# Kernel tuning notes

Hardware: AMD Instinct MI355X
Metric: run time of the kernel (lower is better)

## Reference

```python
import jax, jax.numpy as jnp
import numpy as np
from jax import lax

EPS = 1e-5

def _conv(x, w, b, pad):
    y = lax.conv_general_dilated(x, w, (1, 1), [(pad, pad), (pad, pad)],
                                 dimension_numbers=('NCHW', 'OIHW', 'NCHW'))
    return y + b[None, :, None, None]

def _bn(x, g, b, m, v):
    # eval-mode BatchNorm2d with running stats
    scale = g * lax.rsqrt(v + EPS)
    return x * scale[None, :, None, None] + (b - m * scale)[None, :, None, None]

def setup_inputs() -> dict:
    key = jax.random.key(0)
    ks = jax.random.split(key, 16)
    B, C, H, W = 16, 64, 128, 128
    C2 = 2 * C
    d = {}
    d['x'] = jax.random.normal(ks[0], (B, C, H, W), jnp.float32)
    # fc1: Conv2d(C,C,3,p=1) + BN(C)
    d['fc1_w'] = jax.random.normal(ks[1], (C, C, 3, 3), jnp.float32) * 0.05
    d['fc1_b'] = jax.random.normal(ks[2], (C,), jnp.float32) * 0.05
    d['bn1_g'] = jnp.ones((C,), jnp.float32)
    d['bn1_b'] = jnp.zeros((C,), jnp.float32)
    d['bn1_m'] = jax.random.normal(ks[3], (C,), jnp.float32) * 0.05
    d['bn1_v'] = jax.random.uniform(ks[4], (C,), jnp.float32) * 0.5 + 0.5
    # graph_conv.nn: Conv2d(2C,2C,1) + BN(2C) + GELU
    d['gc_w'] = jax.random.normal(ks[5], (C2, C2, 1, 1), jnp.float32) * 0.05
    d['gc_b'] = jax.random.normal(ks[6], (C2,), jnp.float32) * 0.05
    d['bng_g'] = jnp.ones((C2,), jnp.float32)
    d['bng_b'] = jnp.zeros((C2,), jnp.float32)
    d['bng_m'] = jax.random.normal(ks[7], (C2,), jnp.float32) * 0.05
    d['bng_v'] = jax.random.uniform(ks[8], (C2,), jnp.float32) * 0.5 + 0.5
    # fc2: Conv2d(2C,C,3,p=1) + BN(C)
    d['fc2_w'] = jax.random.normal(ks[9], (C, C2, 3, 3), jnp.float32) * 0.05
    d['fc2_b'] = jax.random.normal(ks[10], (C,), jnp.float32) * 0.05
    d['bn2_g'] = jnp.ones((C,), jnp.float32)
    d['bn2_b'] = jnp.zeros((C,), jnp.float32)
    d['bn2_m'] = jax.random.normal(ks[11], (C,), jnp.float32) * 0.05
    d['bn2_v'] = jax.random.uniform(ks[12], (C,), jnp.float32) * 0.5 + 0.5
    return d

def reference(x, fc1_w, fc1_b, bn1_g, bn1_b, bn1_m, bn1_v,
              gc_w, gc_b, bng_g, bng_b, bng_m, bng_v,
              fc2_w, fc2_b, bn2_g, bn2_b, bn2_m, bn2_v):
    # fc1
    h = _bn(_conv(x, fc1_w, fc1_b, 1), bn1_g, bn1_b, bn1_m, bn1_v)
    # MRConv4dSP: strided self-attention over superpatch tokens
    sel = h[:, :, ::4, ::4]                          # [B,C,h4,w4]
    B, C, h4, w4 = sel.shape
    q = sel.reshape(B, C, h4 * w4).transpose(0, 2, 1)  # [B,N,C]
    scale = C ** (-0.5)
    att = jax.nn.softmax(jnp.einsum('bnc,bmc->bnm', q, q) * scale, axis=-1)
    o = jnp.einsum('bnm,bmc->bnc', att, q)           # [B,N,C]
    o = o.transpose(0, 2, 1).reshape(B, C, h4, w4)
    o = jnp.repeat(jnp.repeat(o, 4, axis=2), 4, axis=3)
    g = jnp.concatenate([h, o], axis=1)              # [B,2C,H,W]
    g = jax.nn.gelu(_bn(_conv(g, gc_w, gc_b, 0), bng_g, bng_b, bng_m, bng_v),
                    approximate=False)
    # fc2 + residual (drop_path=0 -> identity)
    y = _bn(_conv(g, fc2_w, fc2_b, 1), bn2_g, bn2_b, bn2_m, bn2_v)
    return y + x
```

## Files before the change

kernel.cpp:

```cpp
#include <hip/hip_runtime.h>
#include <math.h>

#define EPSV 1e-5f

typedef __bf16 bf16;
using bf16x8 = __attribute__((ext_vector_type(8))) __bf16;
using bf16x4 = __attribute__((ext_vector_type(4))) __bf16;
using bf16x2 = __attribute__((ext_vector_type(2))) __bf16;
using f32x4  = __attribute__((ext_vector_type(4))) float;

static __device__ __forceinline__ f32x4 mfma16(bf16x8 a, bf16x8 b, f32x4 c) {
    return __builtin_amdgcn_mfma_f32_16x16x32_bf16(a, b, c, 0, 0, 0);
}
static __device__ __forceinline__ f32x4 zero4() {
    f32x4 z = {0.f, 0.f, 0.f, 0.f};
    return z;
}

typedef __attribute__((address_space(1))) const char g_char_t;
typedef __attribute__((address_space(3))) char lds_char_t;
static __device__ __forceinline__ void gll16(const void* g, void* l) {
    __builtin_amdgcn_global_load_lds((g_char_t*)g, (lds_char_t*)l, 16, 0, 0);
}

static __device__ __forceinline__ float gelu_f(float v) {
    float z = fabsf(v) * 0.70710678118f;
    float t = __builtin_amdgcn_rcpf(1.f + 0.3275911f * z);
    float poly = t * (0.254829592f + t * (-0.284496736f + t * (1.421413741f +
                 t * (-1.453152027f + t * 1.061405429f))));
    float e = __expf(-z * z);
    float erfv = copysignf(1.f - poly * e, v);
    return 0.5f * v * (1.f + erfv);
}

template<int CIN>
__global__ __launch_bounds__(256) void prep_conv_w(const float* __restrict__ w,
                                                   bf16* __restrict__ wt)
{
    int t = blockIdx.x * 256 + threadIdx.x;
    if (t >= 64 * CIN) return;
    int cout = t / CIN, ci = t - cout * CIN;
    int cci = ci >> 5, lg = (ci >> 3) & 3, j = ci & 7;
    int mi = cout >> 4, lix = cout & 15;
#pragma unroll
    for (int kgt = 0; kgt < 9; ++kgt) {
        float v = w[(size_t)t * 9 + kgt];
        wt[((((size_t)kgt * (CIN >> 5) + cci) * 4 + mi) * 64 + lg * 16 + lix) * 8 + j]
            = (bf16)v;
    }
}

__global__ __launch_bounds__(256) void prep_1x1_w(const float* __restrict__ w,
                                                  bf16* __restrict__ wt)
{
    int t = blockIdx.x * 256 + threadIdx.x;
    int cout = t >> 7, ci = t & 127;
    int ks = ci >> 5, lg = (ci >> 3) & 3, j = ci & 7;
    wt[(((size_t)(ks * 4 + lg) * 128) + cout) * 8 + j] = (bf16)w[t];
}

__global__ __launch_bounds__(256) void cvt_x_nhwc(const float* __restrict__ x,
                                                  bf16* __restrict__ xb,
                                                  float* __restrict__ zb)
{
    __shared__ float t_lds[64 * 68];
    const int bx = blockIdx.x;
    const int b  = blockIdx.y;
    const int y  = bx >> 1, x0 = (bx & 1) * 64;
    const int tid = threadIdx.x;

    if (bx == 0 && b == 0 && tid < 64)
        ((float4*)zb)[tid] = make_float4(0.f, 0.f, 0.f, 0.f);

    for (int f = tid; f < 64 * 16; f += 256) {
        int c = f >> 4, xu = f & 15;
        float4 v = *(const float4*)&x[((size_t)(b * 64 + c) << 14) + (y << 7) + x0 + xu * 4];
        t_lds[(xu * 4 + 0) * 68 + c] = v.x;
        t_lds[(xu * 4 + 1) * 68 + c] = v.y;
        t_lds[(xu * 4 + 2) * 68 + c] = v.z;
        t_lds[(xu * 4 + 3) * 68 + c] = v.w;
    }
    __syncthreads();
    for (int f = tid; f < 64 * 8; f += 256) {
        int xx = f >> 3, cu = f & 7;
        const float* p = &t_lds[xx * 68 + cu * 8];
        bf16x8 v;
#pragma unroll
        for (int j = 0; j < 8; ++j) v[j] = (bf16)p[j];
        *(bf16x8*)&xb[((size_t)((b * 128 + y) * 128) + x0 + xx) * 64 + cu * 8] = v;
    }
}

template<int CIN, int OUTMODE>
__global__ __launch_bounds__(512) void conv3x3_mfma(
    const bf16* __restrict__ in, const bf16* __restrict__ wt,
    const float* __restrict__ bias,
    const float* __restrict__ bg, const float* __restrict__ bb,
    const float* __restrict__ bm, const float* __restrict__ bv,
    const bf16* __restrict__ resid, const bf16* __restrict__ zb,
    void* __restrict__ outp)
{
    constexpr int NC = CIN >> 5;
    __shared__ bf16 in_lds[2][672 * 32];
    __shared__ bf16 w_lds[2][36 * 512];

    const int wg = blockIdx.x;
    const int v  = (wg & 7) * 64 + (wg >> 3);
    const int tile = v & 31, b = v >> 5;
    const int x0 = (tile & 1) * 64;
    const int y0 = (tile >> 1) * 8;
    const int tid  = threadIdx.x;
    const int wid  = tid >> 6;
    const int lane = tid & 63;
    const int lix  = lane & 15, lg = lane >> 4;

    int goff[6]; bool gok[6];
#pragma unroll
    for (int i = 0; i < 6; ++i) {
        int chunk = wid + 8 * i;
        int f = chunk * 64 + lane;
        int pix = f >> 2, u = f & 3;
        int sw = (pix & 3) ^ ((pix >> 2) & 3);
        int ug = u ^ sw;
        int iy = pix / 66, ix = pix - iy * 66;
        int gy = y0 + iy - 1, gx = x0 + ix - 1;
        gok[i]  = (chunk < 42) && (pix < 660) &&
                  (unsigned)gy < 128u && (unsigned)gx < 128u;
        goff[i] = ((b * 128 + gy) * 128 + gx) * CIN + ug * 8;
    }
    int rd[9];
#pragma unroll
    for (int kg = 0; kg < 3; ++kg)
#pragma unroll
        for (int t = 0; t < 3; ++t) {
            int pix0 = (wid + kg) * 66 + lix + t;
            int sw = (pix0 & 3) ^ ((pix0 >> 2) & 3);
            rd[kg * 3 + t] = pix0 * 32 + ((lg ^ sw) << 3);
        }

    f32x4 acc[4][4];
#pragma unroll
    for (int i = 0; i < 4; ++i)
#pragma unroll
        for (int j = 0; j < 4; ++j) acc[i][j] = zero4();

    auto issue_in = [&](int cci, int buf) {
#pragma unroll
        for (int i = 0; i < 6; ++i) {
            int chunk = wid + 8 * i;
            if (chunk < 42) {
                const void* src = gok[i] ? (const void*)(in + goff[i] + cci * 32)
                                         : (const void*)zb;
                gll16(src, (char*)&in_lds[buf][0] + chunk * 1024);
            }
        }
    };
    auto issue_w = [&](int cci, int buf) {
#pragma unroll
        for (int i = 0; i < 5; ++i) {
            int chunk = wid + 8 * i;
            if (chunk < 36) {
                const bf16* src = wt + ((size_t)(chunk >> 2) * NC + cci) * 2048
                                     + (chunk & 3) * 512 + lane * 8;
                gll16(src, (char*)&w_lds[buf][0] + chunk * 1024);
            }
        }
    };
    auto compute = [&](int buf) {
        bf16x8 afA[4], bfA[4], afB[4], bfB[4];
#pragma unroll
        for (int mi = 0; mi < 4; ++mi)
            afA[mi] = *(const bf16x8*)&w_lds[buf][(0 * 4 + mi) * 512 + lane * 8];
#pragma unroll
        for (int nj = 0; nj < 4; ++nj)
            bfA[nj] = *(const bf16x8*)&in_lds[buf][rd[0] + nj * 512];
#pragma unroll
        for (int kgt = 0; kgt < 9; ++kgt) {
            bf16x8* afC = (kgt & 1) ? afB : afA;
            bf16x8* bfC = (kgt & 1) ? bfB : bfA;
            bf16x8* afN = (kgt & 1) ? afA : afB;
            bf16x8* bfN = (kgt & 1) ? bfA : bfB;
            if (kgt < 8) {
#pragma unroll
                for (int mi = 0; mi < 4; ++mi)
                    afN[mi] = *(const bf16x8*)&w_lds[buf][((kgt + 1) * 4 + mi) * 512 + lane * 8];
#pragma unroll
                for (int nj = 0; nj < 4; ++nj)
                    bfN[nj] = *(const bf16x8*)&in_lds[buf][rd[kgt + 1] + nj * 512];
            }
            __builtin_amdgcn_sched_barrier(0);
#pragma unroll
            for (int nj = 0; nj < 4; ++nj)
#pragma unroll
                for (int mi = 0; mi < 4; ++mi)
                    acc[mi][nj] = mfma16(afC[mi], bfC[nj], acc[mi][nj]);
            __builtin_amdgcn_sched_barrier(0);
        }
    };

    issue_in(0, 0);
    issue_w(0, 0);
#pragma unroll 1
    for (int c = 0; c < NC; ++c) {
        if (c + 1 < NC) {
            issue_in(c + 1, (c + 1) & 1);
            issue_w(c + 1, (c + 1) & 1);
            if (wid < 2)      asm volatile("s_waitcnt vmcnt(11)" ::: "memory");
            else if (wid < 4) asm volatile("s_waitcnt vmcnt(10)" ::: "memory");
            else              asm volatile("s_waitcnt vmcnt(9)"  ::: "memory");
        } else {
            asm volatile("s_waitcnt vmcnt(0)" ::: "memory");
        }
        __builtin_amdgcn_s_barrier();
        __builtin_amdgcn_sched_barrier(0);
        compute(c & 1);
        __builtin_amdgcn_s_barrier();
    }

    if (OUTMODE == 0) {
        bf16* out = (bf16*)outp;
        bf16* stg = &in_lds[0][0];
#pragma unroll
        for (int mi = 0; mi < 4; ++mi) {
            float A[4], Bc[4];
#pragma unroll
            for (int r = 0; r < 4; ++r) {
                int c = mi * 16 + lg * 4 + r;
                float s = bg[c] * rsqrtf(bv[c] + EPSV);
                A[r]  = s;
                Bc[r] = bias[c] * s + bb[c] - bm[c] * s;
            }
#pragma unroll
            for (int nj = 0; nj < 4; ++nj) {
                int px = nj * 16 + lix;
                bf16x4 vv;
#pragma unroll
                for (int r = 0; r < 4; ++r)
                    vv[r] = (bf16)(acc[mi][nj][r] * A[r] + Bc[r]);
                *(bf16x4*)&stg[(wid * 64 + px) * 68 + mi * 16 + lg * 4] = vv;
            }
        }
        __syncthreads();
#pragma unroll
        for (int k = 0; k < 8; ++k) {
            int idx = k * 512 + tid;
            int row = idx >> 9, rem = idx & 511;
            int px = rem >> 3, cu = rem & 7;
            bf16x8 vv = *(const bf16x8*)&stg[(row * 64 + px) * 68 + cu * 8];
            *(bf16x8*)&out[((size_t)((b * 128 + y0 + row) * 128)
                            + x0 + px) * 64 + cu * 8] = vv;
        }
    } else {
        float* out = (float*)outp;
        const int gy = y0 + wid;
#pragma unroll
        for (int mi = 0; mi < 4; ++mi) {
            float A[4], Bc[4];
#pragma unroll
            for (int r = 0; r < 4; ++r) {
                int c = mi * 16 + lg * 4 + r;
                float s = bg[c] * rsqrtf(bv[c] + EPSV);
                A[r]  = s;
                Bc[r] = bias[c] * s + bb[c] - bm[c] * s;
            }
#pragma unroll
            for (int nj = 0; nj < 4; ++nj) {
                int px = x0 + nj * 16 + lix;
                bf16x4 rv = *(const bf16x4*)&resid[((size_t)((b * 128 + gy) * 128) + px) * 64
                                                   + mi * 16 + lg * 4];
#pragma unroll
                for (int r = 0; r < 4; ++r) {
                    int c = mi * 16 + lg * 4 + r;
                    size_t oi = ((size_t)(b * 64 + c) << 14) + (gy << 7) + px;
                    out[oi] = acc[mi][nj][r] * A[r] + Bc[r] + (float)rv[r];
                }
            }
        }
    }
}

__global__ __launch_bounds__(256) void gather_q(const bf16* __restrict__ h,
                                                bf16* __restrict__ q)
{
    int t = blockIdx.x * 256 + threadIdx.x;
    int cu = t & 7, n = (t >> 3) & 1023, b = t >> 13;
    int y = (n >> 5) << 2, x = (n & 31) << 2;
    bf16x8 v = *(const bf16x8*)&h[((size_t)((b * 128 + y) * 128 + x)) * 64 + cu * 8];
    *(bf16x8*)&q[((size_t)(b * 1024 + n)) * 64 + cu * 8] = v;
}

__global__ __launch_bounds__(256) void attn_fused(const bf16* __restrict__ q,
                                                  bf16* __restrict__ o)
{
    __shared__ bf16 qn[64 * 72];
    __shared__ bf16 kn[128 * 72];
    __shared__ bf16 vt[64 * 136];
    __shared__ bf16 pl[4][16 * 136];
    __shared__ __align__(16) float fac[4][16];
    const int n0 = blockIdx.x * 64, b = blockIdx.y;
    const int tid = threadIdx.x, w = tid >> 6, lane = tid & 63;
    const int lix = lane & 15, lg = lane >> 4;
    const bf16* qb = q + ((size_t)b << 16);

    for (int f = tid; f < 512; f += 256) {
        int row = f >> 3, cu = f & 7;
        *(bf16x8*)&qn[row * 72 + cu * 8] =
            *(const bf16x8*)&qb[(size_t)(n0 + row) * 64 + cu * 8];
    }

    float m_run = -3.0e38f, l_run = 0.f;
    f32x4 oacc[4];
#pragma unroll
    for (int ct = 0; ct < 4; ++ct) oacc[ct] = zero4();

    for (int mt = 0; mt < 1024; mt += 128) {
        __syncthreads();
        for (int f = tid; f < 1024; f += 256) {
            int row = f >> 3, cu = f & 7;
            *(bf16x8*)&kn[row * 72 + cu * 8] =
                *(const bf16x8*)&qb[(size_t)(mt + row) * 64 + cu * 8];
        }
        for (int f = tid; f < 512; f += 256) {
            int mp = f >> 3, cu = f & 7;
            int m = mp * 2;
            bf16x8 a = *(const bf16x8*)&qb[(size_t)(mt + m) * 64 + cu * 8];
            bf16x8 c = *(const bf16x8*)&qb[(size_t)(mt + m + 1) * 64 + cu * 8];
#pragma unroll
            for (int j = 0; j < 8; ++j) {
                bf16x2 pr = {a[j], c[j]};
                *(bf16x2*)&vt[(cu * 8 + j) * 136 + m] = pr;
            }
        }
        __syncthreads();

        bf16x8 bq0 = *(const bf16x8*)&qn[(w * 16 + lix) * 72 + lg * 8];
        bf16x8 bq1 = *(const bf16x8*)&qn[(w * 16 + lix) * 72 + 32 + lg * 8];

        f32x4 s[8];
#pragma unroll
        for (int t = 0; t < 8; ++t) {
            bf16x8 a0 = *(const bf16x8*)&kn[(t * 16 + lix) * 72 + lg * 8];
            bf16x8 a1 = *(const bf16x8*)&kn[(t * 16 + lix) * 72 + 32 + lg * 8];
            s[t] = mfma16(a0, bq0, zero4());
            s[t] = mfma16(a1, bq1, s[t]);
        }

        float mx = -3.0e38f;
#pragma unroll
        for (int t = 0; t < 8; ++t)
#pragma unroll
            for (int r = 0; r < 4; ++r) { s[t][r] *= 0.125f; mx = fmaxf(mx, s[t][r]); }
        mx = fmaxf(mx, __shfl_xor(mx, 16));
        mx = fmaxf(mx, __shfl_xor(mx, 32));
        float m_new = fmaxf(m_run, mx);
        float alpha = __expf(m_run - m_new);

        float psum = 0.f;
#pragma unroll
        for (int t = 0; t < 8; ++t) {
            float p0 = __expf(s[t][0] - m_new), p1 = __expf(s[t][1] - m_new);
            float p2 = __expf(s[t][2] - m_new), p3 = __expf(s[t][3] - m_new);
            psum += (p0 + p1) + (p2 + p3);
            bf16x2 v01 = {(bf16)p0, (bf16)p1};
            bf16x2 v23 = {(bf16)p2, (bf16)p3};
            *(bf16x2*)&pl[w][lix * 136 + t * 16 + lg * 4]     = v01;
            *(bf16x2*)&pl[w][lix * 136 + t * 16 + lg * 4 + 2] = v23;
        }
        psum += __shfl_xor(psum, 16);
        psum += __shfl_xor(psum, 32);
        l_run = l_run * alpha + psum;
        m_run = m_new;
        if (lg == 0) fac[w][lix] = alpha;

        float4 a4 = *(const float4*)&fac[w][lg * 4];
        float aa[4] = {a4.x, a4.y, a4.z, a4.w};
#pragma unroll
        for (int ct = 0; ct < 4; ++ct)
#pragma unroll
            for (int r = 0; r < 4; ++r) oacc[ct][r] *= aa[r];

#pragma unroll
        for (int kk = 0; kk < 4; ++kk) {
            bf16x8 pa = *(const bf16x8*)&pl[w][lix * 136 + kk * 32 + lg * 8];
#pragma unroll
            for (int ct = 0; ct < 4; ++ct) {
                bf16x8 bv = *(const bf16x8*)&vt[(ct * 16 + lix) * 136 + kk * 32 + lg * 8];
                oacc[ct] = mfma16(pa, bv, oacc[ct]);
            }
        }
    }

    if (lg == 0) fac[w][lix] = l_run;
    float4 l4 = *(const float4*)&fac[w][lg * 4];
    float ll[4] = {1.f / l4.x, 1.f / l4.y, 1.f / l4.z, 1.f / l4.w};
#pragma unroll
    for (int ct = 0; ct < 4; ++ct)
#pragma unroll
        for (int r = 0; r < 4; ++r) {
            int n = n0 + w * 16 + lg * 4 + r;
            int c = ct * 16 + lix;
            o[((size_t)(b * 1024 + n)) * 64 + c] = (bf16)(oacc[ct][r] * ll[r]);
        }
}

__global__ __launch_bounds__(256) void conv1x1_mfma(
    const bf16* __restrict__ h, const bf16* __restrict__ ov,
    const bf16* __restrict__ wt, const float* __restrict__ bias,
    const float* __restrict__ bg, const float* __restrict__ bb,
    const float* __restrict__ bm, const float* __restrict__ bv,
    bf16* __restrict__ g)
{
    __shared__ bf16 in1[128 * 136];
    const int y = blockIdx.x, b = blockIdx.y;
    const int tid = threadIdx.x;
    const int wid = tid >> 6, lane = tid & 63;
    const int lix = lane & 15, lg = lane >> 4;
    const int wm = wid >> 1, wn = wid & 1;

    for (int f = tid; f < 128 * 16; f += 256) {
        int px = f >> 4, cu = f & 15;
        bf16x8 v;
        if (cu < 8) {
            v = *(const bf16x8*)&h[((size_t)((b * 128 + y) * 128 + px)) * 64 + cu * 8];
        } else {
            int n = ((y >> 2) << 5) + (px >> 2);
            v = *(const bf16x8*)&ov[((size_t)(b * 1024 + n)) * 64 + (cu - 8) * 8];
        }
        *(bf16x8*)&in1[px * 136 + cu * 8] = v;
    }
    __syncthreads();

    f32x4 acc[4][4];
#pragma unroll
    for (int i = 0; i < 4; ++i)
#pragma unroll
        for (int j = 0; j < 4; ++j) acc[i][j] = zero4();

#pragma unroll
    for (int ks = 0; ks < 4; ++ks) {
        bf16x8 af[4], bfv[4];
#pragma unroll
        for (int mi = 0; mi < 4; ++mi)
            af[mi] = *(const bf16x8*)&wt[(((size_t)(ks * 4 + lg) * 128) + wm * 64 + mi * 16 + lix) * 8];
#pragma unroll
        for (int nj = 0; nj < 4; ++nj)
            bfv[nj] = *(const bf16x8*)&in1[(wn * 64 + nj * 16 + lix) * 136 + ks * 32 + lg * 8];
#pragma unroll
        for (int mi = 0; mi < 4; ++mi)
#pragma unroll
            for (int nj = 0; nj < 4; ++nj)
                acc[mi][nj] = mfma16(af[mi], bfv[nj], acc[mi][nj]);
    }

    __syncthreads();
    bf16* stg = in1;
#pragma unroll
    for (int mi = 0; mi < 4; ++mi) {
        float A[4], Bc[4];
#pragma unroll
        for (int r = 0; r < 4; ++r) {
            int c = wm * 64 + mi * 16 + lg * 4 + r;
            float s = bg[c] * rsqrtf(bv[c] + EPSV);
            A[r]  = s;
            Bc[r] = bias[c] * s + bb[c] - bm[c] * s;
        }
#pragma unroll
        for (int nj = 0; nj < 4; ++nj) {
            int px = wn * 64 + nj * 16 + lix;
            bf16x4 vv;
#pragma unroll
            for (int r = 0; r < 4; ++r)
                vv[r] = (bf16)gelu_f(acc[mi][nj][r] * A[r] + Bc[r]);
            *(bf16x4*)&stg[px * 132 + wm * 64 + mi * 16 + lg * 4] = vv;
        }
    }
    __syncthreads();
#pragma unroll
    for (int k = 0; k < 8; ++k) {
        int idx = k * 256 + tid;
        int px = idx >> 4, cu = idx & 15;
        bf16x8 v = *(const bf16x8*)&stg[px * 132 + cu * 8];
        *(bf16x8*)&g[((size_t)((b * 128 + y) * 128) + px) * 128 + cu * 8] = v;
    }
}

extern "C" void kernel_launch(void* const* d_in, const int* in_sizes, int n_in,
                              void* d_out, int out_size, void* d_ws, size_t ws_size,
                              hipStream_t stream)
{
    const float* x     = (const float*)d_in[0];
    const float* fc1_w = (const float*)d_in[1];
    const float* fc1_b = (const float*)d_in[2];
    const float* bn1_g = (const float*)d_in[3];
    const float* bn1_b = (const float*)d_in[4];
    const float* bn1_m = (const float*)d_in[5];
    const float* bn1_v = (const float*)d_in[6];
    const float* gc_w  = (const float*)d_in[7];
    const float* gc_b  = (const float*)d_in[8];
    const float* bng_g = (const float*)d_in[9];
    const float* bng_b = (const float*)d_in[10];
    const float* bng_m = (const float*)d_in[11];
    const float* bng_v = (const float*)d_in[12];
    const float* fc2_w = (const float*)d_in[13];
    const float* fc2_b = (const float*)d_in[14];
    const float* bn2_g = (const float*)d_in[15];
    const float* bn2_b = (const float*)d_in[16];
    const float* bn2_m = (const float*)d_in[17];
    const float* bn2_v = (const float*)d_in[18];

    char* wsb = (char*)d_ws;
    bf16* x_bf = (bf16*)wsb;
    bf16* h    = (bf16*)(wsb + 33554432);
    bf16* g    = (bf16*)(wsb + 67108864);
    bf16* q    = (bf16*)(wsb + 134217728);
    bf16* o    = (bf16*)(wsb + 136314880);
    bf16* wt1  = (bf16*)(wsb + 138412032);
    bf16* wt2  = (bf16*)(wsb + 138485760);
    bf16* wtg  = (bf16*)(wsb + 138633216);
    bf16* zb   = (bf16*)(wsb + 138665984);

    prep_conv_w<64><<<16, 256, 0, stream>>>(fc1_w, wt1);
    prep_conv_w<128><<<32, 256, 0, stream>>>(fc2_w, wt2);
    prep_1x1_w<<<64, 256, 0, stream>>>(gc_w, wtg);

    cvt_x_nhwc<<<dim3(256, 16), 256, 0, stream>>>(x, x_bf, (float*)zb);

    conv3x3_mfma<64, 0><<<512, 512, 0, stream>>>(
        x_bf, wt1, fc1_b, bn1_g, bn1_b, bn1_m, bn1_v, nullptr, zb, h);

    gather_q<<<512, 256, 0, stream>>>(h, q);

    attn_fused<<<dim3(16, 16), 256, 0, stream>>>(q, o);

    conv1x1_mfma<<<dim3(128, 16), 256, 0, stream>>>(
        h, o, wtg, gc_b, bng_g, bng_b, bng_m, bng_v, g);

    conv3x3_mfma<128, 1><<<512, 512, 0, stream>>>(
        g, wt2, fc2_b, bn2_g, bn2_b, bn2_m, bn2_v, x_bf, zb, (float*)d_out);
}
```

Before: 185.4 us.

## Merge weight prep kernels and restructure conv3x3 inner loop with per-tap barriers and priority

```diff
diff --git a/kernel.cpp b/kernel.cpp
--- a/kernel.cpp
+++ b/kernel.cpp
@@ -33,12 +33,9 @@
     return 0.5f * v * (1.f + erfv);
 }
 
-template<int CIN>
-__global__ __launch_bounds__(256) void prep_conv_w(const float* __restrict__ w,
-                                                   bf16* __restrict__ wt)
-{
-    int t = blockIdx.x * 256 + threadIdx.x;
-    if (t >= 64 * CIN) return;
+static __device__ __forceinline__ void prep3x3_one(const float* w, bf16* wt,
+                                                   int t, int CIN)
+{
     int cout = t / CIN, ci = t - cout * CIN;
     int cci = ci >> 5, lg = (ci >> 3) & 3, j = ci & 7;
     int mi = cout >> 4, lix = cout & 15;
@@ -50,13 +47,22 @@
     }
 }
 
-__global__ __launch_bounds__(256) void prep_1x1_w(const float* __restrict__ w,
-                                                  bf16* __restrict__ wt)
-{
-    int t = blockIdx.x * 256 + threadIdx.x;
-    int cout = t >> 7, ci = t & 127;
-    int ks = ci >> 5, lg = (ci >> 3) & 3, j = ci & 7;
-    wt[(((size_t)(ks * 4 + lg) * 128) + cout) * 8 + j] = (bf16)w[t];
+__global__ __launch_bounds__(256) void prep_all(
+    const float* __restrict__ fc1_w, const float* __restrict__ fc2_w,
+    const float* __restrict__ gc_w,
+    bf16* __restrict__ wt1, bf16* __restrict__ wt2, bf16* __restrict__ wtg)
+{
+    int bx = blockIdx.x, tid = threadIdx.x;
+    if (bx < 16) {
+        prep3x3_one(fc1_w, wt1, bx * 256 + tid, 64);
+    } else if (bx < 48) {
+        prep3x3_one(fc2_w, wt2, (bx - 16) * 256 + tid, 128);
+    } else {
+        int t = (bx - 48) * 256 + tid;
+        int cout = t >> 7, ci = t & 127;
+        int ks = ci >> 5, lg = (ci >> 3) & 3, j = ci & 7;
+        wtg[(((size_t)(ks * 4 + lg) * 128) + cout) * 8 + j] = (bf16)gc_w[t];
+    }
 }
 
 __global__ __launch_bounds__(256) void cvt_x_nhwc(const float* __restrict__ x,
@@ -167,34 +173,27 @@
         }
     };
     auto compute = [&](int buf) {
-        bf16x8 afA[4], bfA[4], afB[4], bfB[4];
-#pragma unroll
-        for (int mi = 0; mi < 4; ++mi)
-            afA[mi] = *(const bf16x8*)&w_lds[buf][(0 * 4 + mi) * 512 + lane * 8];
-#pragma unroll
-        for (int nj = 0; nj < 4; ++nj)
-            bfA[nj] = *(const bf16x8*)&in_lds[buf][rd[0] + nj * 512];
 #pragma unroll
         for (int kgt = 0; kgt < 9; ++kgt) {
-            bf16x8* afC = (kgt & 1) ? afB : afA;
-            bf16x8* bfC = (kgt & 1) ? bfB : bfA;
-            bf16x8* afN = (kgt & 1) ? afA : afB;
-            bf16x8* bfN = (kgt & 1) ? bfA : bfB;
-            if (kgt < 8) {
+            bf16x8 af[4], bfv[4];
+#pragma unroll
+            for (int mi = 0; mi < 4; ++mi)
+                af[mi] = *(const bf16x8*)&w_lds[buf][(kgt * 4 + mi) * 512 + lane * 8];
+#pragma unroll
+            for (int nj = 0; nj < 4; ++nj)
+                bfv[nj] = *(const bf16x8*)&in_lds[buf][rd[kgt] + nj * 512];
+            __builtin_amdgcn_s_barrier();
+            asm volatile("s_waitcnt lgkmcnt(0)" ::: "memory");
+            __builtin_amdgcn_sched_barrier(0);
+            __builtin_amdgcn_s_setprio(1);
+#pragma unroll
+            for (int nj = 0; nj < 4; ++nj)
 #pragma unroll
                 for (int mi = 0; mi < 4; ++mi)
-                    afN[mi] = *(const bf16x8*)&w_lds[buf][((kgt + 1) * 4 + mi) * 512 + lane * 8];
-#pragma unroll
-                for (int nj = 0; nj < 4; ++nj)
-                    bfN[nj] = *(const bf16x8*)&in_lds[buf][rd[kgt + 1] + nj * 512];
-            }
+                    acc[mi][nj] = mfma16(af[mi], bfv[nj], acc[mi][nj]);
+            __builtin_amdgcn_s_setprio(0);
             __builtin_amdgcn_sched_barrier(0);
-#pragma unroll
-            for (int nj = 0; nj < 4; ++nj)
-#pragma unroll
-                for (int mi = 0; mi < 4; ++mi)
-                    acc[mi][nj] = mfma16(afC[mi], bfC[nj], acc[mi][nj]);
-            __builtin_amdgcn_sched_barrier(0);
+            __builtin_amdgcn_s_barrier();
         }
     };
 
@@ -214,7 +213,6 @@
         __builtin_amdgcn_s_barrier();
         __builtin_amdgcn_sched_barrier(0);
         compute(c & 1);
-        __builtin_amdgcn_s_barrier();
     }
 
     if (OUTMODE == 0) {
@@ -519,9 +517,7 @@
     bf16* wtg  = (bf16*)(wsb + 138633216);
     bf16* zb   = (bf16*)(wsb + 138665984);
 
-    prep_conv_w<64><<<16, 256, 0, stream>>>(fc1_w, wt1);
-    prep_conv_w<128><<<32, 256, 0, stream>>>(fc2_w, wt2);
-    prep_1x1_w<<<64, 256, 0, stream>>>(gc_w, wtg);
+    prep_all<<<112, 256, 0, stream>>>(fc1_w, fc2_w, gc_w, wt1, wt2, wtg);
 
     cvt_x_nhwc<<<dim3(256, 16), 256, 0, stream>>>(x, x_bf, (float*)zb);
 
```

Result: no change. 188.4 us (+1.6%).
